# Performance work log

Hardware: AMD Instinct MI355X
Metric: run time of the kernel (lower is better)

The kernel has to match this reference:

```python
import jax, jax.numpy as jnp
import numpy as np

M, N, D, H, E = 100000, 50000, 128, 2, 1000000
NEG_SLOPE = 0.2  # standard GAT LeakyReLU slope


def setup_inputs() -> dict:
    key = jax.random.key(0)
    ks = jax.random.split(key, 14)
    inp = {
        "u_prev": jax.random.normal(ks[0], (M, D), jnp.float32),
        "i_prev": jax.random.normal(ks[1], (N, D), jnp.float32),
        "w_user": jax.random.normal(ks[2], (D, D), jnp.float32) * 0.05,
        "b_user": jax.random.normal(ks[3], (D,), jnp.float32) * 0.05,
        "w_item": jax.random.normal(ks[4], (D, D), jnp.float32) * 0.05,
        "b_item": jax.random.normal(ks[5], (D,), jnp.float32) * 0.05,
        "a_u_src": jax.random.normal(ks[6], (H, D), jnp.float32) * 0.1,
        "a_u_dst": jax.random.normal(ks[7], (H, D), jnp.float32) * 0.1,
        "a_i_src": jax.random.normal(ks[8], (H, D), jnp.float32) * 0.1,
        "a_i_dst": jax.random.normal(ks[9], (H, D), jnp.float32) * 0.1,
        "u2i_row": jax.random.randint(ks[10], (E,), 0, M, jnp.int32),
        "u2i_col": jax.random.randint(ks[11], (E,), 0, N, jnp.int32),
        "i2u_row": jax.random.randint(ks[12], (E,), 0, N, jnp.int32),
        "i2u_col": jax.random.randint(ks[13], (E,), 0, M, jnp.int32),
    }
    return inp


def _segment_softmax(logits, seg, num_segments):
    # neighborhood softmax: normalize per adjacency row
    mx = jax.ops.segment_max(logits, seg, num_segments=num_segments)
    e = jnp.exp(logits - mx[seg])
    s = jax.ops.segment_sum(e, seg, num_segments=num_segments)
    return e / s[seg]


def _attend(row, col, h_src, h_dst, a_src, a_dst, num_src):
    hs = h_src[row]  # (E, D) gather of source-node features
    hd = h_dst[col]  # (E, D) gather of dest-node features
    head_outs = []
    for h in range(a_src.shape[0]):  # small fixed head count
        logits = jax.nn.leaky_relu(hs @ a_src[h] + hd @ a_dst[h], NEG_SLOPE)  # (E,)
        att = _segment_softmax(logits, row, num_src)                         # (E,)
        # sparse att @ h_dst == row-segment sum of att-weighted neighbor features
        head_outs.append(jax.ops.segment_sum(att[:, None] * hd, row, num_segments=num_src))
    out = sum(head_outs) / len(head_outs)  # reduce_att = mean over heads
    return jax.nn.elu(out)                  # self.nonlinear


def reference(u_prev, i_prev, w_user, b_user, w_item, b_item,
              a_u_src, a_u_dst, a_i_src, a_i_dst,
              u2i_row, u2i_col, i2u_row, i2u_col):
    u = u_prev @ w_user + b_user  # (M, D)
    i = i_prev @ w_item + b_item  # (N, D)
    u_next = _attend(u2i_row, u2i_col, u, i, a_u_src, a_u_dst, M)
    i_next = _attend(i2u_row, i2u_col, i, u, a_i_src, a_i_dst, N)
    return (u_next, i_next)
```

## Files before the change

### kernel.cpp

```cpp
#include <hip/hip_runtime.h>
#include <cstdint>
#include <cstddef>

#define D 128
#define NEG_SLOPE 0.2f
#define CAP 64

__device__ __forceinline__ float lrelu(float x) { return x > 0.0f ? x : NEG_SLOPE * x; }
__device__ __forceinline__ float elu_f(float x) { return x > 0.0f ? x : expm1f(x); }
__device__ __forceinline__ unsigned short f2bf(float f) {
    unsigned u = __float_as_uint(f);
    return (unsigned short)((u + 0x7fffu + ((u >> 16) & 1u)) >> 16);
}

typedef __attribute__((ext_vector_type(8))) short bf16x8;
typedef __attribute__((ext_vector_type(4))) float f32x4;

__global__ __launch_bounds__(256) void prep_w(const float* __restrict__ Wu,
                                              const float* __restrict__ Wi,
                                              unsigned short* __restrict__ WswU,
                                              unsigned short* __restrict__ WswI)
{
    bool di = (int)blockIdx.x >= 8;
    const float* W = di ? Wi : Wu;
    unsigned short* Wsw = di ? WswI : WswU;
    int c = ((int)blockIdx.x & 7) * 256 + (int)threadIdx.x;
    int n = c >> 4, s = c & 15;
    const float* src = W + (size_t)(s * 8) * D + n;
    unsigned t0 = ((unsigned)f2bf(src[0 * D])) | ((unsigned)f2bf(src[1 * D]) << 16);
    unsigned t1 = ((unsigned)f2bf(src[2 * D])) | ((unsigned)f2bf(src[3 * D]) << 16);
    unsigned t2 = ((unsigned)f2bf(src[4 * D])) | ((unsigned)f2bf(src[5 * D]) << 16);
    unsigned t3 = ((unsigned)f2bf(src[6 * D])) | ((unsigned)f2bf(src[7 * D]) << 16);
    *(uint4*)((char*)Wsw + n * 256 + ((s * 16) ^ ((n & 7) << 4))) = make_uint4(t0, t1, t2, t3);
}

struct GemmDir {
    const float* A; const unsigned short* Wsw; const float* bias;
    const float* v0; const float* v1; const float* v2; const float* v3;
    unsigned short* Cb;
    float4* att; int R;
};

__global__ __launch_bounds__(256) void gemm_att(GemmDir g0, int nb0, GemmDir g1)
{
    int gb = blockIdx.x;
    const bool second = gb >= nb0;
    GemmDir g = second ? g1 : g0;
    const int bid = second ? (gb - nb0) : gb;

    __shared__ unsigned short Wl[128 * 128];

    const int tid = threadIdx.x;
    const int wave = tid >> 6;
    const int lane = tid & 63;
    const int lm = lane & 15;
    const int lg = lane >> 4;

    {
        const uint4* wsrc = (const uint4*)g.Wsw;
#pragma unroll
        for (int q = 0; q < 8; ++q) {
            int c = tid + q * 256;
            *(uint4*)((char*)Wl + (size_t)c * 16) = wsrc[c];
        }
    }
    __syncthreads();

    const int xr = (lm & 7) << 4;
    const float* vs[4] = { g.v0, g.v1, g.v2, g.v3 };
    const int colb = lg << 2;

#pragma unroll
    for (int t = 0; t < 2; ++t) {
        const int row0 = bid * 128 + t * 64;
        int ar = row0 + (wave << 4) + lm;
        if (ar > g.R - 1) ar = g.R - 1;
        const float* Arow = g.A + (size_t)ar * D;

        f32x4 acc[8];
#pragma unroll
        for (int nt = 0; nt < 8; ++nt) { acc[nt][0] = 0.f; acc[nt][1] = 0.f; acc[nt][2] = 0.f; acc[nt][3] = 0.f; }

#pragma unroll
        for (int ks = 0; ks < 4; ++ks) {
            const float4 a0 = *(const float4*)(Arow + ks * 32 + lg * 8);
            const float4 a1 = *(const float4*)(Arow + ks * 32 + lg * 8 + 4);
            bf16x8 af;
            af[0] = (short)f2bf(a0.x); af[1] = (short)f2bf(a0.y);
            af[2] = (short)f2bf(a0.z); af[3] = (short)f2bf(a0.w);
            af[4] = (short)f2bf(a1.x); af[5] = (short)f2bf(a1.y);
            af[6] = (short)f2bf(a1.z); af[7] = (short)f2bf(a1.w);
            const int slot = ks * 4 + lg;
            const char* bbase = (const char*)Wl + lm * 256 + ((slot * 16) ^ xr);
#pragma unroll
            for (int nt = 0; nt < 8; ++nt) {
                bf16x8 wf = *(const bf16x8*)(bbase + nt * 4096);
                acc[nt] = __builtin_amdgcn_mfma_f32_16x16x32_bf16(wf, af, acc[nt], 0, 0, 0);
            }
        }

        const int row = row0 + (wave << 4) + lm;
        const bool valid = row < g.R;

#pragma unroll
        for (int nt = 0; nt < 8; ++nt) {
            float4 bv = *(const float4*)(g.bias + nt * 16 + colb);
            acc[nt][0] += bv.x; acc[nt][1] += bv.y; acc[nt][2] += bv.z; acc[nt][3] += bv.w;
        }
        if (valid) {
#pragma unroll
            for (int nt = 0; nt < 8; ++nt) {
                ushort4 s = { f2bf(acc[nt][0]), f2bf(acc[nt][1]), f2bf(acc[nt][2]), f2bf(acc[nt][3]) };
                *(ushort4*)(g.Cb + (size_t)row * D + nt * 16 + colb) = s;
            }
        }

        float p[4];
#pragma unroll
        for (int h = 0; h < 4; ++h) {
            float s = 0.f;
#pragma unroll
            for (int nt = 0; nt < 8; ++nt) {
                float4 vh = *(const float4*)(vs[h] + nt * 16 + colb);
                s += acc[nt][0] * vh.x + acc[nt][1] * vh.y + acc[nt][2] * vh.z + acc[nt][3] * vh.w;
            }
            p[h] = s;
        }
#pragma unroll
        for (int h = 0; h < 4; ++h) {
            p[h] += __shfl_xor(p[h], 16, 64);
            p[h] += __shfl_xor(p[h], 32, 64);
        }
        if (lg == 0 && valid) g.att[row] = make_float4(p[0], p[1], p[2], p[3]);
    }
}

__global__ __launch_bounds__(256) void scatter_fill(
    const int* __restrict__ rowA, const int* __restrict__ colA,
    int* __restrict__ cntA, int* __restrict__ slotA, int EA, int chunkA,
    const int* __restrict__ rowB, const int* __restrict__ colB,
    int* __restrict__ cntB, int* __restrict__ slotB, int EB, int chunkB)
{
    int half = gridDim.x >> 1;
    bool dB = (int)blockIdx.x >= half;
    int b = dB ? (int)blockIdx.x - half : (int)blockIdx.x;
    const int* row = dB ? rowB : rowA;
    const int* col = dB ? colB : colA;
    int* cnt  = dB ? cntB : cntA;
    int* slot = dB ? slotB : slotA;
    int E = dB ? EB : EA;
    int chunk = dB ? chunkB : chunkA;

    int part = b & 7;
    int idx  = b >> 3;
    int nper = half >> 3;
    int lo = part * chunk, hi = lo + chunk;

    for (int i = idx * 256 + (int)threadIdx.x; i < E; i += nper * 256) {
        int r = row[i];
        if (r >= lo && r < hi) {
            int pos = atomicAdd(&cnt[r], 1);
            if (pos < CAP) slot[(size_t)r * CAP + pos] = col[i];
        }
    }
}

__device__ __forceinline__ void aggregate_row(
    const int* __restrict__ cnt, const int* __restrict__ slot,
    const char* __restrict__ satt, const char* __restrict__ datt,
    const unsigned short* __restrict__ featb,
    float* __restrict__ out, int seg, int lane)
{
    int deg = cnt[seg];
    deg = deg > CAP ? CAP : deg;
    float2 sa = *(const float2*)(satt + (size_t)seg * 16);
    float accx = 0.0f, accy = 0.0f;
    if (deg > 0) {
        int myc = 0;
        float e0 = 0.0f, e1 = 0.0f;
        if (lane < deg) {
            myc = slot[(size_t)seg * CAP + lane];
            float2 da = *(const float2*)(datt + (size_t)myc * 16);
            e0 = __expf(lrelu(sa.x + da.x));
            e1 = __expf(lrelu(sa.y + da.y));
        }
        float s0 = e0, s1 = e1;
#pragma unroll
        for (int o = 32; o > 0; o >>= 1) {
            s0 += __shfl_xor(s0, o, 64);
            s1 += __shfl_xor(s1, o, 64);
        }
        float myw = e0 * (0.5f / s0) + e1 * (0.5f / s1);
        float a0x = 0.f, a0y = 0.f, a1x = 0.f, a1y = 0.f,
              a2x = 0.f, a2y = 0.f, a3x = 0.f, a3y = 0.f;
        int j = 0;
        for (; j + 4 <= deg; j += 4) {
            int c0 = __shfl(myc, j, 64), c1 = __shfl(myc, j + 1, 64);
            int c2 = __shfl(myc, j + 2, 64), c3 = __shfl(myc, j + 3, 64);
            float w0 = __shfl(myw, j, 64), w1 = __shfl(myw, j + 1, 64);
            float w2 = __shfl(myw, j + 2, 64), w3 = __shfl(myw, j + 3, 64);
            unsigned f0 = *(const unsigned*)(featb + (size_t)c0 * D + 2 * lane);
            unsigned f1 = *(const unsigned*)(featb + (size_t)c1 * D + 2 * lane);
            unsigned f2 = *(const unsigned*)(featb + (size_t)c2 * D + 2 * lane);
            unsigned f3 = *(const unsigned*)(featb + (size_t)c3 * D + 2 * lane);
            a0x += w0 * __uint_as_float(f0 << 16); a0y += w0 * __uint_as_float(f0 & 0xffff0000u);
            a1x += w1 * __uint_as_float(f1 << 16); a1y += w1 * __uint_as_float(f1 & 0xffff0000u);
            a2x += w2 * __uint_as_float(f2 << 16); a2y += w2 * __uint_as_float(f2 & 0xffff0000u);
            a3x += w3 * __uint_as_float(f3 << 16); a3y += w3 * __uint_as_float(f3 & 0xffff0000u);
        }
        for (; j < deg; ++j) {
            int c0 = __shfl(myc, j, 64);
            float w0 = __shfl(myw, j, 64);
            unsigned f0 = *(const unsigned*)(featb + (size_t)c0 * D + 2 * lane);
            a0x += w0 * __uint_as_float(f0 << 16); a0y += w0 * __uint_as_float(f0 & 0xffff0000u);
        }
        accx = (a0x + a1x) + (a2x + a3x);
        accy = (a0y + a1y) + (a2y + a3y);
    }
    *(float2*)(out + (size_t)seg * D + 2 * lane) = make_float2(elu_f(accx), elu_f(accy));
}

__global__ __launch_bounds__(256) void aggregate_both(
    const int* cntA, const int* slotA, const char* sattA, const char* dattA,
    const unsigned short* featA, float* outA, int SA, int nbA,
    const int* cntB, const int* slotB, const char* sattB, const char* dattB,
    const unsigned short* featB, float* outB, int SB)
{
    int lane = threadIdx.x & 63;
    if (blockIdx.x < (unsigned)nbA) {
        int seg = blockIdx.x * 4 + (threadIdx.x >> 6);
        if (seg < SA) aggregate_row(cntA, slotA, sattA, dattA, featA, outA, seg, lane);
    } else {
        int seg = (blockIdx.x - nbA) * 4 + (threadIdx.x >> 6);
        if (seg < SB) aggregate_row(cntB, slotB, sattB, dattB, featB, outB, seg, lane);
    }
}

extern "C" void kernel_launch(void* const* d_in, const int* in_sizes, int n_in,
                              void* d_out, int out_size, void* d_ws, size_t ws_size,
                              hipStream_t stream)
{
    const float* u_prev  = (const float*)d_in[0];
    const float* i_prev  = (const float*)d_in[1];
    const float* w_user  = (const float*)d_in[2];
    const float* b_user  = (const float*)d_in[3];
    const float* w_item  = (const float*)d_in[4];
    const float* b_item  = (const float*)d_in[5];
    const float* a_u_src = (const float*)d_in[6];
    const float* a_u_dst = (const float*)d_in[7];
    const float* a_i_src = (const float*)d_in[8];
    const float* a_i_dst = (const float*)d_in[9];
    const int* u2i_row = (const int*)d_in[10];
    const int* u2i_col = (const int*)d_in[11];
    const int* i2u_row = (const int*)d_in[12];
    const int* i2u_col = (const int*)d_in[13];

    const int M = in_sizes[0] / D;
    const int N = in_sizes[1] / D;
    const int EA = in_sizes[10];
    const int EB = in_sizes[12];

    char* ws = (char*)d_ws;
    size_t off = 0;
    auto carve = [&](size_t bytes) -> char* {
        char* p = ws + off;
        off += (bytes + 255) & ~(size_t)255;
        return p;
    };
    unsigned short* u_featb = (unsigned short*)carve((size_t)M * D * 2);
    unsigned short* i_featb = (unsigned short*)carve((size_t)N * D * 2);
    float4* u_att   = (float4*)carve((size_t)M * 16);
    float4* i_att   = (float4*)carve((size_t)N * 16);
    int*    cntA    = (int*)carve((size_t)M * 4);
    int*    cntB    = (int*)carve((size_t)N * 4);
    int*    slotA   = (int*)carve((size_t)M * CAP * 4);
    int*    slotB   = (int*)carve((size_t)N * CAP * 4);
    unsigned short* wswU = (unsigned short*)carve((size_t)D * D * 2);
    unsigned short* wswI = (unsigned short*)carve((size_t)D * D * 2);
    (void)ws_size; (void)n_in; (void)out_size;

    hipMemsetAsync(cntA, 0, (size_t)M * 4, stream);
    hipMemsetAsync(cntB, 0, (size_t)N * 4, stream);

    prep_w<<<16, 256, 0, stream>>>(w_user, w_item, wswU, wswI);

    GemmDir gu = { u_prev, wswU, b_user, a_u_src, a_u_src + D, a_i_dst, a_i_dst + D, u_featb, u_att, M };
    GemmDir gi = { i_prev, wswI, b_item, a_u_dst, a_u_dst + D, a_i_src, a_i_src + D, i_featb, i_att, N };
    int nbGu = (M + 127) / 128, nbGi = (N + 127) / 128;
    gemm_att<<<nbGu + nbGi, 256, 0, stream>>>(gu, nbGu, gi);

    int chunkA = (M + 7) / 8, chunkB = (N + 7) / 8;
    scatter_fill<<<2048, 256, 0, stream>>>(u2i_row, u2i_col, cntA, slotA, EA, chunkA,
                                           i2u_row, i2u_col, cntB, slotB, EB, chunkB);

    float* out_u = (float*)d_out;
    float* out_i = out_u + (size_t)M * D;
    int nbAggA = (M + 3) / 4, nbAggB = (N + 3) / 4;
    aggregate_both<<<nbAggA + nbAggB, 256, 0, stream>>>(
        cntA, slotA, (const char*)u_att, (const char*)i_att, i_featb, out_u, M, nbAggA,
        cntB, slotB, (const char*)i_att + 8, (const char*)u_att + 8, u_featb, out_i, N);
}
```

Baseline: 395.1 us.

## Fold counter zeroing into weight prep kernel and widen GEMM blocks to 512 threads

The two memset calls are replaced by extra blocks in the weight-swizzle kernel, which now zero the per-row counters with vector stores, removing two launches. The GEMM+attention kernel moves to 512-thread blocks that each cover 256 rows, so the 32KB shared-memory weight tile is loaded once per 256 rows instead of once per 128. This halves the weight staging traffic and block count but raises per-block register and LDS pressure and may lower occupancy. The zeroing covers M>>2 and N>>2 int4s, which relies on M and N being multiples of 4.

New measurement: 396.2 us. About the same (+0.3%).

```diff
diff --git a/kernel.cpp b/kernel.cpp
--- a/kernel.cpp
+++ b/kernel.cpp
@@ -16,22 +16,34 @@
 typedef __attribute__((ext_vector_type(8))) short bf16x8;
 typedef __attribute__((ext_vector_type(4))) float f32x4;
 
-__global__ __launch_bounds__(256) void prep_w(const float* __restrict__ Wu,
-                                              const float* __restrict__ Wi,
-                                              unsigned short* __restrict__ WswU,
-                                              unsigned short* __restrict__ WswI)
-{
-    bool di = (int)blockIdx.x >= 8;
-    const float* W = di ? Wi : Wu;
-    unsigned short* Wsw = di ? WswI : WswU;
-    int c = ((int)blockIdx.x & 7) * 256 + (int)threadIdx.x;
-    int n = c >> 4, s = c & 15;
-    const float* src = W + (size_t)(s * 8) * D + n;
-    unsigned t0 = ((unsigned)f2bf(src[0 * D])) | ((unsigned)f2bf(src[1 * D]) << 16);
-    unsigned t1 = ((unsigned)f2bf(src[2 * D])) | ((unsigned)f2bf(src[3 * D]) << 16);
-    unsigned t2 = ((unsigned)f2bf(src[4 * D])) | ((unsigned)f2bf(src[5 * D]) << 16);
-    unsigned t3 = ((unsigned)f2bf(src[6 * D])) | ((unsigned)f2bf(src[7 * D]) << 16);
-    *(uint4*)((char*)Wsw + n * 256 + ((s * 16) ^ ((n & 7) << 4))) = make_uint4(t0, t1, t2, t3);
+__global__ __launch_bounds__(256) void prep_w_zero(
+    const float* __restrict__ Wu, const float* __restrict__ Wi,
+    unsigned short* __restrict__ WswU, unsigned short* __restrict__ WswI,
+    int* __restrict__ cntA, int M, int* __restrict__ cntB, int N)
+{
+    int b = (int)blockIdx.x;
+    if (b < 16) {
+        bool di = b >= 8;
+        const float* W = di ? Wi : Wu;
+        unsigned short* Wsw = di ? WswI : WswU;
+        int c = (b & 7) * 256 + (int)threadIdx.x;
+        int n = c >> 4, s = c & 15;
+        const float* src = W + (size_t)(s * 8) * D + n;
+        unsigned t0 = ((unsigned)f2bf(src[0 * D])) | ((unsigned)f2bf(src[1 * D]) << 16);
+        unsigned t1 = ((unsigned)f2bf(src[2 * D])) | ((unsigned)f2bf(src[3 * D]) << 16);
+        unsigned t2 = ((unsigned)f2bf(src[4 * D])) | ((unsigned)f2bf(src[5 * D]) << 16);
+        unsigned t3 = ((unsigned)f2bf(src[6 * D])) | ((unsigned)f2bf(src[7 * D]) << 16);
+        *(uint4*)((char*)Wsw + n * 256 + ((s * 16) ^ ((n & 7) << 4))) = make_uint4(t0, t1, t2, t3);
+        return;
+    }
+    int nA4 = M >> 2, nB4 = N >> 2;
+    int total4 = nA4 + nB4;
+    int stride = ((int)gridDim.x - 16) * 256;
+    int4 z = make_int4(0, 0, 0, 0);
+    for (int j = (b - 16) * 256 + (int)threadIdx.x; j < total4; j += stride) {
+        if (j < nA4) ((int4*)cntA)[j] = z;
+        else ((int4*)cntB)[j - nA4] = z;
+    }
 }
 
 struct GemmDir {
@@ -41,7 +53,7 @@
     float4* att; int R;
 };
 
-__global__ __launch_bounds__(256) void gemm_att(GemmDir g0, int nb0, GemmDir g1)
+__global__ __launch_bounds__(512) void gemm_att(GemmDir g0, int nb0, GemmDir g1)
 {
     int gb = blockIdx.x;
     const bool second = gb >= nb0;
@@ -59,8 +71,8 @@
     {
         const uint4* wsrc = (const uint4*)g.Wsw;
 #pragma unroll
-        for (int q = 0; q < 8; ++q) {
-            int c = tid + q * 256;
+        for (int q = 0; q < 4; ++q) {
+            int c = tid + q * 512;
             *(uint4*)((char*)Wl + (size_t)c * 16) = wsrc[c];
         }
     }
@@ -72,8 +84,8 @@
 
 #pragma unroll
     for (int t = 0; t < 2; ++t) {
-        const int row0 = bid * 128 + t * 64;
-        int ar = row0 + (wave << 4) + lm;
+        const int rowbase = bid * 256 + t * 128 + wave * 16;
+        int ar = rowbase + lm;
         if (ar > g.R - 1) ar = g.R - 1;
         const float* Arow = g.A + (size_t)ar * D;
 
@@ -99,7 +111,7 @@
             }
         }
 
-        const int row = row0 + (wave << 4) + lm;
+        const int row = rowbase + lm;
         const bool valid = row < g.R;
 
 #pragma unroll
@@ -279,15 +291,13 @@
     unsigned short* wswI = (unsigned short*)carve((size_t)D * D * 2);
     (void)ws_size; (void)n_in; (void)out_size;
 
-    hipMemsetAsync(cntA, 0, (size_t)M * 4, stream);
-    hipMemsetAsync(cntB, 0, (size_t)N * 4, stream);
-
-    prep_w<<<16, 256, 0, stream>>>(w_user, w_item, wswU, wswI);
+    prep_w_zero<<<16 + 160, 256, 0, stream>>>(w_user, w_item, wswU, wswI,
+                                              cntA, M, cntB, N);
 
     GemmDir gu = { u_prev, wswU, b_user, a_u_src, a_u_src + D, a_i_dst, a_i_dst + D, u_featb, u_att, M };
     GemmDir gi = { i_prev, wswI, b_item, a_u_dst, a_u_dst + D, a_i_src, a_i_src + D, i_featb, i_att, N };
-    int nbGu = (M + 127) / 128, nbGi = (N + 127) / 128;
-    gemm_att<<<nbGu + nbGi, 256, 0, stream>>>(gu, nbGu, gi);
+    int nbGu = (M + 255) / 256, nbGi = (N + 255) / 256;
+    gemm_att<<<nbGu + nbGi, 512, 0, stream>>>(gu, nbGu, gi);
 
     int chunkA = (M + 7) / 8, chunkB = (N + 7) / 8;
     scatter_fill<<<2048, 256, 0, stream>>>(u2i_row, u2i_col, cntA, slotA, EA, chunkA,
```
